# Performance work log

Hardware: AMD Instinct MI355X
Metric: run time of the kernel (lower is better)

The kernel has to match this reference:

```python
import jax, jax.numpy as jnp
import numpy as np

B, CIN, COUT, H, W, K = 32, 256, 256, 56, 56, 3
STRIDE, PAD, DIL = 1, 1, 1
SPARSITY = 0.9  # fraction of weight entries pruned to zero


def setup_inputs() -> dict:
    key = jax.random.key(0)
    kx, kw, km = jax.random.split(key, 3)
    x = jax.random.normal(kx, (B, CIN, H, W), dtype=jnp.float32)
    w = jax.random.normal(kw, (COUT, CIN, K, K), dtype=jnp.float32)
    mask = (jax.random.uniform(km, (COUT, CIN, K, K)) > SPARSITY).astype(jnp.float32)
    w = w * mask
    return {"x": x, "weight": w}


def reference(x, weight):
    # Faithful math of SparseConv2D.forward (sparse path == nn.Conv2d, bias=None):
    # NCHW input, OIHW weight, stride/pad/dilation as configured.
    out = jax.lax.conv_general_dilated(
        x, weight,
        window_strides=(STRIDE, STRIDE),
        padding=[(PAD, PAD), (PAD, PAD)],
        rhs_dilation=(DIL, DIL),
        dimension_numbers=("NCHW", "OIHW", "NCHW"),
    )
    return out  # [B, COUT, H_out, W_out]
```

## Files before the change

kernel.cpp:

```cpp
#include <hip/hip_runtime.h>


typedef __attribute__((ext_vector_type(8))) short short8;
typedef __attribute__((ext_vector_type(4))) float f32x4;
typedef __attribute__((ext_vector_type(4))) int i32x4;

constexpr int BB = 32, CIN = 256, COUT = 256, H = 56, W = 56, HW = H * W;
constexpr int HP = 58, WP = 58;

constexpr size_t XP_ELEMS = (size_t)BB * HP * WP * CIN;
constexpr size_t WB_ELEMS = (size_t)COUT * 9 * CIN;
constexpr size_t WS_NEEDED = (XP_ELEMS + WB_ELEMS) * 2;

__device__ __forceinline__ ushort f2bf(float f) {
    unsigned x = __float_as_uint(f);
    unsigned r = (x + 0x7FFFu + ((x >> 16) & 1u)) >> 16;
    return (ushort)r;
}


__global__ __launch_bounds__(256)
void prep_xp(const float* __restrict__ x, ushort* __restrict__ xp) {
    const int bi = blockIdx.x;
    const int b = bi / HP, i = bi % HP;
    ushort* dst = xp + (size_t)bi * WP * CIN;
    const int tid = threadIdx.x;

    if (i == 0 || i == HP - 1) {
        i32x4 z = {0, 0, 0, 0};
        for (int k = tid; k < WP * CIN / 8; k += 256) ((i32x4*)dst)[k] = z;
        return;
    }

    __shared__ ushort t[W][CIN + 2];
    const int lane = tid & 63, wv = tid >> 6;
    if (lane < W) {
        const float* src = x + (size_t)b * CIN * HW + (size_t)(i - 1) * W + lane;
        for (int cin = wv; cin < CIN; cin += 4)
            t[lane][cin] = f2bf(src[(size_t)cin * HW]);
    }
    __syncthreads();
    for (int c = 0; c < WP; ++c)
        dst[c * CIN + tid] = (c == 0 || c == WP - 1) ? (ushort)0 : t[c - 1][tid];
}

__global__ __launch_bounds__(256)
void prep_wb2(const float* __restrict__ w, ushort* __restrict__ wb2) {
    const int d = blockIdx.x * 256 + threadIdx.x;
    const int ci = d & 31;
    const int cout = (d >> 5) & 255;
    const int r = d >> 13;
    const int tap = r % 9, cb = r / 9;
    const int cin = cb * 32 + ci;
    wb2[d] = f2bf(w[((size_t)cout * CIN + cin) * 9 + tap]);
}


#define SCHED_FENCE() __builtin_amdgcn_sched_barrier(0)
#define WAITV0 asm volatile("s_waitcnt vmcnt(0)" ::: "memory")
#define WAITV4 asm volatile("s_waitcnt vmcnt(4)" ::: "memory")
#define WAITV8 asm volatile("s_waitcnt vmcnt(8)" ::: "memory")

__device__ __forceinline__ void gload_lds16(const ushort* g, ushort* l) {
    __builtin_amdgcn_global_load_lds(
        (const __attribute__((address_space(1))) void*)g,
        (__attribute__((address_space(3))) void*)l, 16, 0, 0);
}

__device__ __forceinline__ int swz(int c) { return c ^ ((c >> 3) & 7); }

__global__ __launch_bounds__(256, 2)
void conv_mfma(const ushort* __restrict__ xp, const ushort* __restrict__ wb2,
               float* __restrict__ out) {
    int bx = blockIdx.x;
    bx = (bx & 7) * 112 + (bx >> 3);

    const int b  = bx / 28;
    const int p0 = (bx % 28) * 112;
    const int r0 = p0 / 56;

    const int tid  = threadIdx.x;
    const int wv   = tid >> 6;
    const int lane = tid & 63;
    const int ml   = lane & 15;
    const int g    = lane >> 4;

    __shared__ ushort As[2][8192];
    __shared__ ushort Xs[2][8192];

    int aoffB[4];
    #pragma unroll
    for (int mi = 0; mi < 4; ++mi)
        aoffB[mi] = swz((64 * wv + 16 * mi + ml) * 4 + g) * 16;
    int cbase[7];
    #pragma unroll
    for (int nf = 0; nf < 7; ++nf) {
        const int p_  = p0 + 16 * nf + ml;
        const int hl  = (p_ >= p0 + 56) ? 1 : 0;
        const int col = p_ - 56 * (r0 + hl);
        cbase[nf] = (hl * 58 + col) * 4 + g;
    }
    int goffA[4], goffX[4];
    #pragma unroll
    for (int k = 0; k < 4; ++k) {
        const int q = k * 256 + tid;
        const int c = swz(q);
        goffA[k] = (c >> 2) * 32 + (c & 3) * 8;
        goffX[k] = (c < 928) ? ((c >> 2) * 256 + (c & 3) * 8) : 0;
    }
    const size_t xbase = ((size_t)b * HP + r0) * WP * CIN;

    f32x4 acc[4][7] = {};

    #define STAGE_A(SLAB, BUF)                                                  \
        { const ushort* _s = wb2 + (size_t)(SLAB) * 8192;                       \
          _Pragma("unroll")                                                     \
          for (int k = 0; k < 4; ++k)                                           \
              gload_lds16(_s + goffA[k], &As[BUF][(k * 256 + wv * 64) * 8]); }
    #define STAGE_X(CB, BUF)                                                    \
        { const ushort* _s = xp + xbase + (CB) * 32;                            \
          _Pragma("unroll")                                                     \
          for (int k = 0; k < 4; ++k)                                           \
              gload_lds16(_s + goffX[k], &Xs[BUF][(k * 256 + wv * 64) * 8]); }

    STAGE_X(0, 0);
    STAGE_A(0, 0);
    STAGE_A(1, 1);
    WAITV4;
    __syncthreads();

    const int DSLOT[9] = {0, 1, 2, 58, 59, 60, 116, 117, 118};

    #pragma unroll
    for (int cb = 0; cb < 8; ++cb) {
        #pragma unroll
        for (int tap = 0; tap < 9; ++tap) {
            const int t = cb * 9 + tap;

            if (tap == 8 && cb < 7) { WAITV8; } else { WAITV4; }
            SCHED_FENCE();
            __builtin_amdgcn_s_barrier();
            SCHED_FENCE();

            const ushort* Ab = &As[t & 1][0];
            const ushort* Xb = &Xs[cb & 1][0];

            short8 av[4], bv[7];
            #pragma unroll
            for (int mi = 0; mi < 4; ++mi)
                av[mi] = *(const short8*)((const char*)Ab + aoffB[mi]);
            #pragma unroll
            for (int nf = 0; nf < 7; ++nf) {
                const int c = cbase[nf] + 4 * DSLOT[tap];
                bv[nf] = *(const short8*)((const char*)Xb + swz(c) * 16);
            }

            __builtin_amdgcn_s_setprio(1);
            #pragma unroll
            for (int mi = 0; mi < 4; ++mi)
                #pragma unroll
                for (int nf = 0; nf < 7; ++nf)
                    acc[mi][nf] = __builtin_amdgcn_mfma_f32_16x16x32_bf16(
                                      av[mi], bv[nf], acc[mi][nf], 0, 0, 0);
            __builtin_amdgcn_s_setprio(0);
            SCHED_FENCE();
            __builtin_amdgcn_s_barrier();
            SCHED_FENCE();

            {
                int slab = t + 2;
                if (slab >= 72) slab -= 72;
                STAGE_A(slab, t & 1);
            }
            if (tap == 7 && cb < 7) STAGE_X(cb + 1, (cb + 1) & 1);
            SCHED_FENCE();
        }
    }
    WAITV0;

    float* ob = out + (size_t)b * COUT * HW;
    #pragma unroll
    for (int mi = 0; mi < 4; ++mi)
        #pragma unroll
        for (int nf = 0; nf < 7; ++nf)
            #pragma unroll
            for (int r = 0; r < 4; ++r) {
                const int cout_l = 64 * wv + 16 * mi + 4 * g + r;
                const int p_ = p0 + 16 * nf + ml;
                ob[(size_t)cout_l * HW + p_] = acc[mi][nf][r];
            }
    #undef STAGE_A
    #undef STAGE_X
}


constexpr int WSZ = CIN * 9;
constexpr int NIN = 54 * 54;

__global__ __launch_bounds__(256)
void sparse_conv3x3(const float* __restrict__ x,
                    const float* __restrict__ wgt,
                    float* __restrict__ out) {
    const int bc = blockIdx.x, cout = bc % COUT, b = bc / COUT;
    const int tid = threadIdx.x;
    __shared__ int2 s_ent[WSZ];
    __shared__ unsigned char s_kk[WSZ];
    __shared__ int s_cnt[257];
    const float* wc = wgt + (size_t)cout * WSZ;
    float mv[9]; int cnt = 0;
    #pragma unroll
    for (int i = 0; i < 9; ++i) { mv[i] = wc[tid * 9 + i]; if (mv[i] != 0.0f) cnt++; }
    s_cnt[tid] = cnt; __syncthreads();
    if (tid == 0) { int run = 0; for (int t = 0; t < 256; ++t) { int c = s_cnt[t]; s_cnt[t] = run; run += c; } s_cnt[256] = run; }
    __syncthreads();
    { int pos = s_cnt[tid];
      #pragma unroll
      for (int i = 0; i < 9; ++i) if (mv[i] != 0.0f) {
          const int kh = i / 3, kw = i - kh * 3;
          int2 e; e.x = (tid * HW + (kh - 1) * W + (kw - 1)) * 4; e.y = __float_as_int(mv[i]);
          s_ent[pos] = e; s_kk[pos] = (unsigned char)(kh | (kw << 4)); pos++; } }
    __syncthreads();
    const int nnz = s_cnt[256];
    const char* xb = (const char*)(x + (size_t)b * CIN * HW);
    float* ob = out + (size_t)bc * HW;
    for (int o = tid; o < HW; o += 256) {
        int h, w; bool interior = (o < NIN);
        if (interior) { h = 1 + o / 54; w = 1 + (o - (h - 1) * 54); }
        else { int o2 = o - NIN;
            if (o2 < 56) { h = 0; w = o2; } else if (o2 < 112) { h = 55; w = o2 - 56; }
            else if (o2 < 166) { h = 1 + (o2 - 112); w = 0; } else { h = 1 + (o2 - 166); w = 55; } }
        const char* pb = xb + (size_t)(h * W + w) * 4;
        float acc = 0.0f;
        if (interior) {
            #pragma unroll 4
            for (int e = 0; e < nnz; ++e) { const int2 en = s_ent[e];
                acc = fmaf(__int_as_float(en.y), *(const float*)(pb + en.x), acc); }
        } else {
            const int h1 = h - 1, w1 = w - 1;
            for (int e = 0; e < nnz; ++e) { const int2 en = s_ent[e]; const int kk = s_kk[e];
                const int hh = h1 + (kk & 15), ww = w1 + (kk >> 4);
                if ((unsigned)hh < (unsigned)H && (unsigned)ww < (unsigned)W)
                    acc = fmaf(__int_as_float(en.y), *(const float*)(pb + en.x), acc); } }
        ob[h * W + w] = acc;
    }
}


extern "C" void kernel_launch(void* const* d_in, const int* in_sizes, int n_in,
                              void* d_out, int out_size, void* d_ws, size_t ws_size,
                              hipStream_t stream) {
    const float* x = (const float*)d_in[0];
    const float* w = (const float*)d_in[1];
    float* out = (float*)d_out;

    if (ws_size >= WS_NEEDED) {
        ushort* xp = (ushort*)d_ws;
        ushort* wbp = xp + XP_ELEMS;
        prep_xp<<<BB * HP, 256, 0, stream>>>(x, xp);
        prep_wb2<<<(int)(WB_ELEMS / 256), 256, 0, stream>>>(w, wbp);
        conv_mfma<<<896, 256, 0, stream>>>(xp, wbp, out);
    } else {
        sparse_conv3x3<<<BB * COUT, 256, 0, stream>>>(x, w, out);
    }
}
```

Before: 153.5 us.

## Single-buffer the input tile and restage it row-by-row as taps finish

Replaces the double-buffered X tile in LDS with a single buffer laid out as four 256-chunk rows. Each row is refilled with the next channel block as soon as the taps that read it are done. This halves X shared memory, which could allow higher occupancy, and spreads the X loads across the tap loop. The cost is finer-grained vmcnt waits, a non-unrolled outer cb loop, and a tighter dependency on the ordering between row reuse and refill.

```diff
diff --git a/kernel.cpp b/kernel.cpp
--- a/kernel.cpp
+++ b/kernel.cpp
@@ -59,7 +59,8 @@
 #define SCHED_FENCE() __builtin_amdgcn_sched_barrier(0)
 #define WAITV0 asm volatile("s_waitcnt vmcnt(0)" ::: "memory")
 #define WAITV4 asm volatile("s_waitcnt vmcnt(4)" ::: "memory")
-#define WAITV8 asm volatile("s_waitcnt vmcnt(8)" ::: "memory")
+#define WAITV5 asm volatile("s_waitcnt vmcnt(5)" ::: "memory")
+#define WAITV6 asm volatile("s_waitcnt vmcnt(6)" ::: "memory")
 
 __device__ __forceinline__ void gload_lds16(const ushort* g, ushort* l) {
     __builtin_amdgcn_global_load_lds(
@@ -85,8 +86,8 @@
     const int ml   = lane & 15;
     const int g    = lane >> 4;
 
-    __shared__ ushort As[2][8192];
-    __shared__ ushort Xs[2][8192];
+    __shared__ ushort As0[8192], As1[8192];
+    __shared__ ushort Xs[8192];
 
     int aoffB[4];
     #pragma unroll
@@ -98,15 +99,18 @@
         const int p_  = p0 + 16 * nf + ml;
         const int hl  = (p_ >= p0 + 56) ? 1 : 0;
         const int col = p_ - 56 * (r0 + hl);
-        cbase[nf] = (hl * 58 + col) * 4 + g;
-    }
-    int goffA[4], goffX[4];
+        cbase[nf] = hl * 256 + col * 4 + g;
+    }
+    int goffA[4];
     #pragma unroll
     for (int k = 0; k < 4; ++k) {
-        const int q = k * 256 + tid;
-        const int c = swz(q);
+        const int c = swz(k * 256 + tid);
         goffA[k] = (c >> 2) * 32 + (c & 3) * 8;
-        goffX[k] = (c < 928) ? ((c >> 2) * 256 + (c & 3) * 8) : 0;
+    }
+    int xoff;
+    {
+        const int ii = (tid & 0xC0) | ((tid & 63) ^ (((tid & 63) >> 3) & 7));
+        xoff = (ii < 232) ? ((ii >> 2) * CIN + (ii & 3) * 8) : 0;
     }
     const size_t xbase = ((size_t)b * HP + r0) * WP * CIN;
 
@@ -116,34 +120,31 @@
         { const ushort* _s = wb2 + (size_t)(SLAB) * 8192;                       \
           _Pragma("unroll")                                                     \
           for (int k = 0; k < 4; ++k)                                           \
-              gload_lds16(_s + goffA[k], &As[BUF][(k * 256 + wv * 64) * 8]); }
-    #define STAGE_X(CB, BUF)                                                    \
-        { const ushort* _s = xp + xbase + (CB) * 32;                            \
-          _Pragma("unroll")                                                     \
-          for (int k = 0; k < 4; ++k)                                           \
-              gload_lds16(_s + goffX[k], &Xs[BUF][(k * 256 + wv * 64) * 8]); }
-
-    STAGE_X(0, 0);
-    STAGE_A(0, 0);
-    STAGE_A(1, 1);
-    WAITV4;
-    __syncthreads();
-
-    const int DSLOT[9] = {0, 1, 2, 58, 59, 60, 116, 117, 118};
-
-    #pragma unroll
+              gload_lds16(_s + goffA[k], &(BUF)[(k * 256 + wv * 64) * 8]); }
+    #define STAGE_XROW(RR, CBN)                                                 \
+        gload_lds16(xp + xbase + (size_t)(RR) * WP * CIN + (CBN) * 32 + xoff,   \
+                    &Xs[((RR) * 256 + wv * 64) * 8])
+
+    STAGE_XROW(0, 0); STAGE_XROW(1, 0); STAGE_XROW(2, 0); STAGE_XROW(3, 0);
+    STAGE_A(0, As0);
+    STAGE_A(1, As1);
+    WAITV0;
+    __syncthreads();
+
     for (int cb = 0; cb < 8; ++cb) {
+        const int par = cb & 1;
+        const int cbn = (cb < 7) ? cb + 1 : 0;
         #pragma unroll
         for (int tap = 0; tap < 9; ++tap) {
-            const int t = cb * 9 + tap;
-
-            if (tap == 8 && cb < 7) { WAITV8; } else { WAITV4; }
+            if      (tap == 0 || tap == 1) { WAITV6; }
+            else if (tap == 2 || tap == 5 || tap == 8) { WAITV4; }
+            else                            { WAITV5; }
             SCHED_FENCE();
             __builtin_amdgcn_s_barrier();
             SCHED_FENCE();
 
-            const ushort* Ab = &As[t & 1][0];
-            const ushort* Xb = &Xs[cb & 1][0];
+            const ushort* Ab = (par ^ (tap & 1)) ? As1 : As0;
+            const int kh = tap / 3, kw = tap - kh * 3;
 
             short8 av[4], bv[7];
             #pragma unroll
@@ -151,8 +152,8 @@
                 av[mi] = *(const short8*)((const char*)Ab + aoffB[mi]);
             #pragma unroll
             for (int nf = 0; nf < 7; ++nf) {
-                const int c = cbase[nf] + 4 * DSLOT[tap];
-                bv[nf] = *(const short8*)((const char*)Xb + swz(c) * 16);
+                const int c = cbase[nf] + kh * 256 + kw * 4;
+                bv[nf] = *(const short8*)((const char*)Xs + swz(c) * 16);
             }
 
             __builtin_amdgcn_s_setprio(1);
@@ -168,11 +169,14 @@
             SCHED_FENCE();
 
             {
-                int slab = t + 2;
-                if (slab >= 72) slab -= 72;
-                STAGE_A(slab, t & 1);
+                int t2 = cb * 9 + tap + 2;
+                if (t2 >= 72) t2 -= 72;
+                ushort* abuf = (par ^ (tap & 1)) ? As1 : As0;
+                STAGE_A(t2, abuf);
             }
-            if (tap == 7 && cb < 7) STAGE_X(cb + 1, (cb + 1) & 1);
+            if (tap == 2) { STAGE_XROW(0, cbn); }
+            else if (tap == 5) { STAGE_XROW(1, cbn); }
+            else if (tap == 8) { STAGE_XROW(2, cbn); STAGE_XROW(3, cbn); }
             SCHED_FENCE();
         }
     }
@@ -190,7 +194,7 @@
                 ob[(size_t)cout_l * HW + p_] = acc[mi][nf][r];
             }
     #undef STAGE_A
-    #undef STAGE_X
+    #undef STAGE_XROW
 }
 
 
```

Result: slower. 173.6 us (+13.1%).

## Stage three weight taps per barrier phase to cut synchronization count

Applied to the files above, without the earlier changes.

The weight staging is regrouped so that each pipeline phase loads three tap slabs (one kernel row) into a triple-sized LDS buffer, and the MFMA loop processes three taps between barriers. This cuts the number of barrier pairs per K sweep from 72 to 24 and deepens the outstanding global loads, with the vmcnt waits raised to match. In exchange, LDS use grows to about 128KB per block, which may limit occupancy to one block per CU despite the launch bound of 2. The X buffer is now also prefetched on the last channel block, which wastes one redundant load.

```diff
diff --git a/kernel.cpp b/kernel.cpp
--- a/kernel.cpp
+++ b/kernel.cpp
@@ -57,9 +57,9 @@
 
 
 #define SCHED_FENCE() __builtin_amdgcn_sched_barrier(0)
-#define WAITV0 asm volatile("s_waitcnt vmcnt(0)" ::: "memory")
-#define WAITV4 asm volatile("s_waitcnt vmcnt(4)" ::: "memory")
-#define WAITV8 asm volatile("s_waitcnt vmcnt(8)" ::: "memory")
+#define WAITV0  asm volatile("s_waitcnt vmcnt(0)"  ::: "memory")
+#define WAITV12 asm volatile("s_waitcnt vmcnt(12)" ::: "memory")
+#define WAITV16 asm volatile("s_waitcnt vmcnt(16)" ::: "memory")
 
 __device__ __forceinline__ void gload_lds16(const ushort* g, ushort* l) {
     __builtin_amdgcn_global_load_lds(
@@ -85,8 +85,8 @@
     const int ml   = lane & 15;
     const int g    = lane >> 4;
 
-    __shared__ ushort As[2][8192];
-    __shared__ ushort Xs[2][8192];
+    __shared__ ushort As0[3 * 8192], As1[3 * 8192];
+    __shared__ ushort Xs0[8192], Xs1[8192];
 
     int aoffB[4];
     #pragma unroll
@@ -112,67 +112,75 @@
 
     f32x4 acc[4][7] = {};
 
-    #define STAGE_A(SLAB, BUF)                                                  \
-        { const ushort* _s = wb2 + (size_t)(SLAB) * 8192;                       \
+    #define STAGE_A3(PH, BUF)                                                   \
+        { int _s0 = (PH) * 3; if (_s0 >= 72) _s0 -= 72;                         \
           _Pragma("unroll")                                                     \
-          for (int k = 0; k < 4; ++k)                                           \
-              gload_lds16(_s + goffA[k], &As[BUF][(k * 256 + wv * 64) * 8]); }
+          for (int s = 0; s < 3; ++s) {                                         \
+              const ushort* _src = wb2 + (size_t)(_s0 + s) * 8192;              \
+              _Pragma("unroll")                                                 \
+              for (int k = 0; k < 4; ++k)                                       \
+                  gload_lds16(_src + goffA[k],                                  \
+                              (BUF) + s * 8192 + (k * 256 + wv * 64) * 8);      \
+          } }
     #define STAGE_X(CB, BUF)                                                    \
         { const ushort* _s = xp + xbase + (CB) * 32;                            \
           _Pragma("unroll")                                                     \
           for (int k = 0; k < 4; ++k)                                           \
-              gload_lds16(_s + goffX[k], &Xs[BUF][(k * 256 + wv * 64) * 8]); }
-
-    STAGE_X(0, 0);
-    STAGE_A(0, 0);
-    STAGE_A(1, 1);
-    WAITV4;
-    __syncthreads();
-
-    const int DSLOT[9] = {0, 1, 2, 58, 59, 60, 116, 117, 118};
-
-    #pragma unroll
+              gload_lds16(_s + goffX[k], (BUF) + (k * 256 + wv * 64) * 8); }
+
+    STAGE_X(0, Xs0);
+    STAGE_A3(0, As0);
+    STAGE_A3(1, As1);
+    WAITV0;
+    __syncthreads();
+
     for (int cb = 0; cb < 8; ++cb) {
         #pragma unroll
-        for (int tap = 0; tap < 9; ++tap) {
-            const int t = cb * 9 + tap;
-
-            if (tap == 8 && cb < 7) { WAITV8; } else { WAITV4; }
+        for (int q = 0; q < 3; ++q) {
+            const int ph = cb * 3 + q;
+
+            if (q == 2) { WAITV16; } else { WAITV12; }
             SCHED_FENCE();
             __builtin_amdgcn_s_barrier();
             SCHED_FENCE();
 
-            const ushort* Ab = &As[t & 1][0];
-            const ushort* Xb = &Xs[cb & 1][0];
-
-            short8 av[4], bv[7];
+            const ushort* Ab = (ph & 1) ? As1 : As0;
+            const ushort* Xb = (cb & 1) ? Xs1 : Xs0;
+
             #pragma unroll
-            for (int mi = 0; mi < 4; ++mi)
-                av[mi] = *(const short8*)((const char*)Ab + aoffB[mi]);
-            #pragma unroll
-            for (int nf = 0; nf < 7; ++nf) {
-                const int c = cbase[nf] + 4 * DSLOT[tap];
-                bv[nf] = *(const short8*)((const char*)Xb + swz(c) * 16);
-            }
-
-            __builtin_amdgcn_s_setprio(1);
-            #pragma unroll
-            for (int mi = 0; mi < 4; ++mi)
+            for (int kw = 0; kw < 3; ++kw) {
+                short8 av[4], bv[7];
                 #pragma unroll
-                for (int nf = 0; nf < 7; ++nf)
-                    acc[mi][nf] = __builtin_amdgcn_mfma_f32_16x16x32_bf16(
-                                      av[mi], bv[nf], acc[mi][nf], 0, 0, 0);
-            __builtin_amdgcn_s_setprio(0);
+                for (int mi = 0; mi < 4; ++mi)
+                    av[mi] = *(const short8*)((const char*)Ab + kw * 16384 + aoffB[mi]);
+                #pragma unroll
+                for (int nf = 0; nf < 7; ++nf) {
+                    const int c = cbase[nf] + 4 * (q * 58 + kw);
+                    bv[nf] = *(const short8*)((const char*)Xb + swz(c) * 16);
+                }
+                __builtin_amdgcn_s_setprio(1);
+                #pragma unroll
+                for (int mi = 0; mi < 4; ++mi)
+                    #pragma unroll
+                    for (int nf = 0; nf < 7; ++nf)
+                        acc[mi][nf] = __builtin_amdgcn_mfma_f32_16x16x32_bf16(
+                                          av[mi], bv[nf], acc[mi][nf], 0, 0, 0);
+                __builtin_amdgcn_s_setprio(0);
+            }
             SCHED_FENCE();
             __builtin_amdgcn_s_barrier();
             SCHED_FENCE();
 
             {
-                int slab = t + 2;
-                if (slab >= 72) slab -= 72;
-                STAGE_A(slab, t & 1);
-            }
-            if (tap == 7 && cb < 7) STAGE_X(cb + 1, (cb + 1) & 1);
+                int phn = ph + 2;
+                if (phn >= 24) phn -= 24;
+                ushort* abuf = (ph & 1) ? As1 : As0;
+                STAGE_A3(phn, abuf);
+            }
+            if (q == 1) {
+                const int cbn = (cb < 7) ? cb + 1 : 0;
+                STAGE_X(cbn, (cb & 1) ? Xs0 : Xs1);
+            }
             SCHED_FENCE();
         }
     }
@@ -189,7 +197,7 @@
                 const int p_ = p0 + 16 * nf + ml;
                 ob[(size_t)cout_l * HW + p_] = acc[mi][nf][r];
             }
-    #undef STAGE_A
+    #undef STAGE_A3
     #undef STAGE_X
 }
 
```

New measurement: 199.4 us. 29.9% more time.
